# Performance work log

Measured on AMD Instinct MI355X. Metric: run time of the kernel, lower is better.

Reference implementation:

```python
import jax, jax.numpy as jnp
import numpy as np

D_MODEL = 1024
NHEADS = 16
E_HEAD = D_MODEL // NHEADS  # 64
ROPE_BASE = 10000.0


def _rope_cos_sin(L, dim, base, dtype):
    # dim = E_head (even); inv_freq over pairs, GPT-NeoX half-split convention
    inv_freq = 1.0 / (base ** (jnp.arange(0, dim, 2, dtype=jnp.float32) / dim))
    pos = jnp.arange(L, dtype=jnp.float32)
    freqs = pos[:, None] * inv_freq[None, :]  # [L, dim/2]
    return jnp.cos(freqs).astype(dtype), jnp.sin(freqs).astype(dtype)


def _apply_rope(t, cos, sin):
    # t: [B, H, L, Dh]; rotate-half formulation
    d2 = t.shape[-1] // 2
    t1, t2 = t[..., :d2], t[..., d2:]
    return jnp.concatenate([t1 * cos - t2 * sin, t1 * sin + t2 * cos], axis=-1)


def setup_inputs() -> dict:
    key = jax.random.key(0)
    ks = jax.random.split(key, 5)
    B, L = 4, 2048
    x = jax.random.normal(ks[0], (B, L, D_MODEL), dtype=jnp.float32)
    s_in = 1.0 / np.sqrt(D_MODEL)
    W_packed = jax.random.normal(ks[1], (3 * D_MODEL, D_MODEL), dtype=jnp.float32) * s_in
    b_packed = jax.random.normal(ks[2], (3 * D_MODEL,), dtype=jnp.float32) * 0.02
    W_out = jax.random.normal(ks[3], (D_MODEL, D_MODEL), dtype=jnp.float32) * s_in
    b_out = jax.random.normal(ks[4], (D_MODEL,), dtype=jnp.float32) * 0.02
    return {"x": x, "W_packed": W_packed, "b_packed": b_packed, "W_out": W_out, "b_out": b_out}


def reference(x, W_packed, b_packed, W_out, b_out):
    B, L, _ = x.shape
    # 1) packed QKV projection (query is key is value path)
    qkv = jnp.einsum('ble,fe->blf', x, W_packed) + b_packed  # [B, L, 3*D]
    q, k, v = jnp.split(qkv, 3, axis=-1)
    # 2) split heads -> [B, H, L, Dh]
    def heads(t):
        return t.reshape(B, L, NHEADS, E_HEAD).transpose(0, 2, 1, 3)
    q, k, v = heads(q), heads(k), heads(v)
    # 3) RoPE on q, k
    cos, sin = _rope_cos_sin(L, E_HEAD, ROPE_BASE, x.dtype)
    q = _apply_rope(q, cos, sin)
    k = _apply_rope(k, cos, sin)
    # 4) SDPA (non-causal, no dropout)
    scale = 1.0 / np.sqrt(E_HEAD)
    scores = jnp.einsum('bhqd,bhkd->bhqk', q, k) * scale
    attn = jax.nn.softmax(scores, axis=-1)
    out = jnp.einsum('bhqk,bhkd->bhqd', attn, v)
    # 5) merge heads + output projection
    out = out.transpose(0, 2, 1, 3).reshape(B, L, D_MODEL)
    return jnp.einsum('bld,ed->ble', out, W_out) + b_out
```

## Files before the change

kernel.cpp:

```cpp
#include <hip/hip_runtime.h>
#include <hip/hip_bf16.h>
#include <stdint.h>

#define L_SEQ 2048
#define NB    4
#define NH    16
#define EH    64
#define DM    1024
#define MTOT  (NB * L_SEQ)

typedef __attribute__((ext_vector_type(8))) short bf16x8;
typedef __attribute__((ext_vector_type(4))) float f32x4;
typedef __attribute__((ext_vector_type(16))) float f32x16;

static __device__ __forceinline__ float bf2f(short u) {
    union { unsigned int i; float f; } c;
    c.i = ((unsigned int)(unsigned short)u) << 16;
    return c.f;
}
static __device__ __forceinline__ short f2bf(float f) {
    union { float f; unsigned int i; } c; c.f = f;
    unsigned int x = c.i;
    unsigned int r = (x + 0x7fffu + ((x >> 16) & 1u)) >> 16;
    return (short)(unsigned short)r;
}
static __device__ __forceinline__ unsigned cvtpk(float lo, float hi) {
    unsigned r;
    asm volatile("v_cvt_pk_bf16_f32 %0, %1, %2" : "=v"(r) : "v"(lo), "v"(hi));
    return r;
}

static __device__ __forceinline__ void gload_lds16(const void* g, void* lds) {
    __builtin_amdgcn_global_load_lds(
        (const __attribute__((address_space(1))) unsigned int*)g,
        (__attribute__((address_space(3))) unsigned int*)lds, 16, 0, 0);
}

__global__ __launch_bounds__(256) void cvt3_k(const float* __restrict__ x,
                                              const float* __restrict__ wp,
                                              const float* __restrict__ wo,
                                              short* __restrict__ xb,
                                              short* __restrict__ wpb,
                                              short* __restrict__ wob,
                                              float* __restrict__ tab) {
    int bid = blockIdx.x;
    if (bid >= 12288) {
        int i = (bid - 12288) * 256 + threadIdx.x;
        int l = i >> 5, d = i & 31;
        float inv = powf(10000.0f, -(float)d * (1.0f / 32.0f));
        float fr = (float)l * inv;
        tab[i]         = cosf(fr);
        tab[65536 + i] = sinf(fr);
        return;
    }
    const float* src; short* dst; int i;
    if (bid < 8192)       { src = x;  dst = xb;  i = bid * 256 + threadIdx.x; }
    else if (bid < 11264) { src = wp; dst = wpb; i = (bid - 8192) * 256 + threadIdx.x; }
    else                  { src = wo; dst = wob; i = (bid - 11264) * 256 + threadIdx.x; }
    float4 v = ((const float4*)src)[i];
    short4 o;
    o.x = f2bf(v.x); o.y = f2bf(v.y); o.z = f2bf(v.z); o.w = f2bf(v.w);
    ((short4*)dst)[i] = o;
}

template<int OUTBF16, int NBN, int NCOL>
__global__ __launch_bounds__(512, 2) void gemmA_k(const short* __restrict__ A,
                                                  const short* __restrict__ Bt,
                                                  const float* __restrict__ bias,
                                                  void* __restrict__ Cv) {
    __shared__ short lds[2][384 * 32];
    const int t = threadIdx.x;
    const int w = t >> 6, l = t & 63;
    const int wm = w >> 1, wn = w & 1;
    const int lr = l & 15, lh = l >> 4;

    const int nblk = NBN * 32;
    int fid = blockIdx.x + blockIdx.y * NBN;
    int swz = (fid & 7) * (nblk >> 3) + (fid >> 3);
    const int n0 = (swz % NBN) * 128;
    const int m0 = (swz / NBN) * 256;

    const int lrow = l >> 2;
    const int schunk = (l & 3) ^ ((l >> 3) & 3);

    const short* Ag = A + (size_t)(m0 + lrow) * 1024 + schunk * 8;
    const short* Bg = Bt + (size_t)(n0 + lrow) * 1024 + schunk * 8;

    auto STAGE = [&](int kt, int buf) {
        gload_lds16(Ag + (size_t)(w * 32) * 1024 + kt * 32,      &lds[buf][(w * 32) * 32]);
        gload_lds16(Ag + (size_t)(w * 32 + 16) * 1024 + kt * 32, &lds[buf][(w * 32 + 16) * 32]);
        gload_lds16(Bg + (size_t)(w * 16) * 1024 + kt * 32,      &lds[buf][8192 + (w * 16) * 32]);
    };

    f32x4 acc[4][4] = {};

    STAGE(0, 0);
    STAGE(1, 1);
    asm volatile("s_waitcnt vmcnt(3)" ::: "memory");
    __builtin_amdgcn_s_barrier();

    const int fch = (lh ^ ((lr >> 1) & 3)) << 3;

#pragma unroll 2
    for (int kt = 0; kt < 32; ++kt) {
        const int c = kt & 1;
        const short* Al = &lds[c][0];
        const short* Bl = &lds[c][8192];

        bf16x8 bfr[4], af[4];
#pragma unroll
        for (int nj = 0; nj < 4; ++nj)
            bfr[nj] = *(const bf16x8*)(Bl + (wn * 64 + nj * 16 + lr) * 32 + fch);
#pragma unroll
        for (int mi = 0; mi < 4; ++mi)
            af[mi] = *(const bf16x8*)(Al + (wm * 64 + mi * 16 + lr) * 32 + fch);

        __builtin_amdgcn_s_setprio(1);
#pragma unroll
        for (int mi = 0; mi < 4; ++mi)
#pragma unroll
            for (int nj = 0; nj < 4; ++nj)
                acc[mi][nj] = __builtin_amdgcn_mfma_f32_16x16x32_bf16(
                    af[mi], bfr[nj], acc[mi][nj], 0, 0, 0);
        __builtin_amdgcn_s_setprio(0);

        asm volatile("s_waitcnt lgkmcnt(0)" ::: "memory");
        __builtin_amdgcn_s_barrier();
        if (kt + 2 < 32) {
            STAGE(kt + 2, c);
            asm volatile("s_waitcnt vmcnt(3)" ::: "memory");
        } else {
            asm volatile("s_waitcnt vmcnt(0)" ::: "memory");
        }
        __builtin_amdgcn_s_barrier();
    }

#pragma unroll
    for (int mi = 0; mi < 4; ++mi) {
#pragma unroll
        for (int nj = 0; nj < 4; ++nj) {
            const int row = m0 + wm * 64 + mi * 16 + lh * 4;
            const int col = n0 + wn * 64 + nj * 16 + lr;
            const float bsv = bias[col];
#pragma unroll
            for (int j = 0; j < 4; ++j) {
                float v = acc[mi][nj][j] + bsv;
                if (OUTBF16)
                    ((short*)Cv)[(size_t)(row + j) * NCOL + col] = f2bf(v);
                else
                    ((float*)Cv)[(size_t)(row + j) * NCOL + col] = v;
            }
        }
    }
}

__global__ __launch_bounds__(256) void scatter_k(const short* __restrict__ qkv,
                                                 const float* __restrict__ tab,
                                                 short* __restrict__ Q,
                                                 short* __restrict__ Kd,
                                                 short* __restrict__ Vt) {
    int bid = blockIdx.x;
    if (bid < 4096) {
        int idx = bid * 256 + threadIdx.x;
        int dp = (idx & 7) * 4;
        int h = (idx >> 3) & 15;
        int bl = idx >> 7;
        int l = bl & (L_SEQ - 1);
        int b = bl >> 11;
        float4 cs = *(const float4*)&tab[l * 32 + dp];
        float4 sn = *(const float4*)&tab[65536 + l * 32 + dp];
        const short* row = qkv + (size_t)bl * 3072;
        size_t ob = ((size_t)((b * 16 + h) * 2048 + l)) * 64;
        const float sc = 0.18033688011112042f;
        short4 q1 = *(const short4*)&row[h * 64 + dp];
        short4 q2 = *(const short4*)&row[h * 64 + dp + 32];
        union { unsigned u[2]; short4 s4; } a1, a2;
        a1.u[0] = cvtpk((bf2f(q1.x) * cs.x - bf2f(q2.x) * sn.x) * sc,
                        (bf2f(q1.y) * cs.y - bf2f(q2.y) * sn.y) * sc);
        a1.u[1] = cvtpk((bf2f(q1.z) * cs.z - bf2f(q2.z) * sn.z) * sc,
                        (bf2f(q1.w) * cs.w - bf2f(q2.w) * sn.w) * sc);
        a2.u[0] = cvtpk((bf2f(q1.x) * sn.x + bf2f(q2.x) * cs.x) * sc,
                        (bf2f(q1.y) * sn.y + bf2f(q2.y) * cs.y) * sc);
        a2.u[1] = cvtpk((bf2f(q1.z) * sn.z + bf2f(q2.z) * cs.z) * sc,
                        (bf2f(q1.w) * sn.w + bf2f(q2.w) * cs.w) * sc);
        *(short4*)(Q + ob + dp)      = a1.s4;
        *(short4*)(Q + ob + dp + 32) = a2.s4;
        short4 k1 = *(const short4*)&row[1024 + h * 64 + dp];
        short4 k2 = *(const short4*)&row[1024 + h * 64 + dp + 32];
        union { unsigned u[2]; short4 s4; } e1, e2;
        e1.u[0] = cvtpk(bf2f(k1.x) * cs.x - bf2f(k2.x) * sn.x,
                        bf2f(k1.y) * cs.y - bf2f(k2.y) * sn.y);
        e1.u[1] = cvtpk(bf2f(k1.z) * cs.z - bf2f(k2.z) * sn.z,
                        bf2f(k1.w) * cs.w - bf2f(k2.w) * sn.w);
        e2.u[0] = cvtpk(bf2f(k1.x) * sn.x + bf2f(k2.x) * cs.x,
                        bf2f(k1.y) * sn.y + bf2f(k2.y) * cs.y);
        e2.u[1] = cvtpk(bf2f(k1.z) * sn.z + bf2f(k2.z) * cs.z,
                        bf2f(k1.w) * sn.w + bf2f(k2.w) * cs.w);
        int r7 = l & 7;
        int c1 = ((dp >> 3) ^ r7) * 8 + (dp & 7);
        int c2 = (((dp >> 3) | 4) ^ r7) * 8 + (dp & 7);
        *(short4*)(Kd + ob + c1) = e1.s4;
        *(short4*)(Kd + ob + c2) = e2.s4;
        return;
    }
    __shared__ short tile[64 * 65];
    int bid2 = bid - 4096;
    int l0 = (bid2 & 31) * 64;
    int bh = bid2 >> 5;
    int t = threadIdx.x;
    int b = bh >> 4, h = bh & 15;
#pragma unroll
    for (int i = 0; i < 16; i++) {
        int l = i * 4 + (t >> 6);
        int d = t & 63;
        tile[d * 65 + l] = qkv[(size_t)(b * 2048 + l0 + l) * 3072 + 2048 + h * 64 + d];
    }
    __syncthreads();
#pragma unroll
    for (int i = 0; i < 16; i++) {
        int d = i * 4 + (t >> 6);
        int lx = t & 63;
        int cl = (lx & ~0xC) | ((lx & 4) << 1) | ((lx & 8) >> 1);
        int lp = l0 | ((((cl >> 3) ^ (d & 7)) << 3)) | (cl & 7);
        Vt[(size_t)(bh * 64 + d) * 2048 + lp] = tile[d * 65 + lx];
    }
}

__global__ __launch_bounds__(512, 2) void attn_k(const short* __restrict__ Qg,
                                                 const short* __restrict__ Kg,
                                                 const short* __restrict__ Vt,
                                                 short* __restrict__ O) {
    __shared__ short Ks[3][64 * 64];
    __shared__ short Vs[3][64 * 64];
    const int t = threadIdx.x;
    const int w = t >> 6, l = t & 63;
    const int q = l & 31, hi = l >> 5;
    const int r7 = l & 7;

    const int od = blockIdx.x + blockIdx.y * 8;
    const int qblk = (od >> 3) & 7;
    const int bh = (od & 7) * 8 + (od >> 6);
    const int q0 = qblk * 256;

    const short* Qb = Qg + (size_t)bh * (2048 * 64);
    const short* Kb = Kg + (size_t)bh * (2048 * 64);
    const short* Vb = Vt + (size_t)bh * (64 * 2048);

    const int qrow = q0 + w * 32 + q;
    bf16x8 qf[4];
#pragma unroll
    for (int ds = 0; ds < 4; ds++)
        qf[ds] = *(const bf16x8*)(Qb + (size_t)qrow * 64 + ds * 16 + hi * 8);

    const short one_bf = (short)0x3F80;
    const bf16x8 ones = {one_bf, one_bf, one_bf, one_bf, one_bf, one_bf, one_bf, one_bf};

    f32x16 o0 = {}, o1 = {}, os = {};

    const int grow = w * 8 + (l >> 3);
    const int gcol = r7 * 8;

    gload_lds16(Kb + (size_t)grow * 64 + gcol,        &Ks[0][w * 512]);
    gload_lds16(Vb + (size_t)grow * 2048 + gcol,      &Vs[0][w * 512]);
    gload_lds16(Kb + (size_t)(64 + grow) * 64 + gcol, &Ks[1][w * 512]);
    gload_lds16(Vb + (size_t)grow * 2048 + 64 + gcol, &Vs[1][w * 512]);
    asm volatile("s_waitcnt vmcnt(2)" ::: "memory");
    __builtin_amdgcn_s_barrier();

    const short* Kc = &Ks[0][0];  const short* Vc = &Vs[0][0];
    const short* Kn = &Ks[1][0];  const short* Vn = &Vs[1][0];
    short*       Kf = &Ks[2][0];  short*       Vf = &Vs[2][0];

    for (int it = 0; it < 32; ++it) {
        if (it < 30) {
            const int kn = (it + 2) * 64;
            gload_lds16(Kb + (size_t)(kn + grow) * 64 + gcol, Kf + w * 512);
            gload_lds16(Vb + (size_t)grow * 2048 + kn + gcol, Vf + w * 512);
        }

        f32x16 s0 = {}, s1 = {};
#pragma unroll
        for (int ds = 0; ds < 4; ds++) {
            const int ch = ((ds << 1) | hi) ^ r7;
            bf16x8 k0f = *(const bf16x8*)(Kc + q * 64 + ch * 8);
            bf16x8 k1f = *(const bf16x8*)(Kc + (32 + q) * 64 + ch * 8);
            __builtin_amdgcn_s_setprio(1);
            s0 = __builtin_amdgcn_mfma_f32_32x32x16_bf16(k0f, qf[ds], s0, 0, 0, 0);
            s1 = __builtin_amdgcn_mfma_f32_32x32x16_bf16(k1f, qf[ds], s1, 0, 0, 0);
            __builtin_amdgcn_s_setprio(0);
        }

#pragma unroll
        for (int r = 0; r < 16; r++) {
            s0[r] = __builtin_amdgcn_exp2f(s0[r]);
            s1[r] = __builtin_amdgcn_exp2f(s1[r]);
        }

        bf16x8 pf[4];
        {
            union { unsigned u[4]; bf16x8 v; } f;
            f.u[0] = cvtpk(s0[0], s0[1]);  f.u[1] = cvtpk(s0[2], s0[3]);
            f.u[2] = cvtpk(s0[4], s0[5]);  f.u[3] = cvtpk(s0[6], s0[7]);
            pf[0] = f.v;
            f.u[0] = cvtpk(s0[8], s0[9]);  f.u[1] = cvtpk(s0[10], s0[11]);
            f.u[2] = cvtpk(s0[12], s0[13]); f.u[3] = cvtpk(s0[14], s0[15]);
            pf[1] = f.v;
            f.u[0] = cvtpk(s1[0], s1[1]);  f.u[1] = cvtpk(s1[2], s1[3]);
            f.u[2] = cvtpk(s1[4], s1[5]);  f.u[3] = cvtpk(s1[6], s1[7]);
            pf[2] = f.v;
            f.u[0] = cvtpk(s1[8], s1[9]);  f.u[1] = cvtpk(s1[10], s1[11]);
            f.u[2] = cvtpk(s1[12], s1[13]); f.u[3] = cvtpk(s1[14], s1[15]);
            pf[3] = f.v;
        }

#pragma unroll
        for (int ks = 0; ks < 4; ks++) {
            const int ch = ((ks << 1) | hi) ^ r7;
            bf16x8 v0f = *(const bf16x8*)(Vc + q * 64 + ch * 8);
            bf16x8 v1f = *(const bf16x8*)(Vc + (32 + q) * 64 + ch * 8);
            __builtin_amdgcn_s_setprio(1);
            o0 = __builtin_amdgcn_mfma_f32_32x32x16_bf16(v0f, pf[ks], o0, 0, 0, 0);
            o1 = __builtin_amdgcn_mfma_f32_32x32x16_bf16(v1f, pf[ks], o1, 0, 0, 0);
            os = __builtin_amdgcn_mfma_f32_32x32x16_bf16(ones, pf[ks], os, 0, 0, 0);
            __builtin_amdgcn_s_setprio(0);
        }

        asm volatile("s_waitcnt lgkmcnt(0)" ::: "memory");
        if (it < 30) asm volatile("s_waitcnt vmcnt(2)" ::: "memory");
        else         asm volatile("s_waitcnt vmcnt(0)" ::: "memory");
        __builtin_amdgcn_s_barrier();

        const short* tk = Kc; Kc = Kn; Kn = Kf; Kf = (short*)tk;
        const short* tv = Vc; Vc = Vn; Vn = Vf; Vf = (short*)tv;
    }

    const float inv = 1.0f / os[0];
    const int b = bh >> 4, h = bh & 15;
    short* Orow = O + (size_t)(b * 2048 + qrow) * 1024 + h * 64;
#pragma unroll
    for (int g = 0; g < 4; g++) {
        unsigned w0 = cvtpk(o0[g * 4 + 0] * inv, o0[g * 4 + 1] * inv);
        unsigned w1 = cvtpk(o0[g * 4 + 2] * inv, o0[g * 4 + 3] * inv);
        unsigned long long p0 = (unsigned long long)w0 | ((unsigned long long)w1 << 32);
        *(unsigned long long*)(Orow + g * 8 + hi * 4) = p0;
        unsigned w2 = cvtpk(o1[g * 4 + 0] * inv, o1[g * 4 + 1] * inv);
        unsigned w3 = cvtpk(o1[g * 4 + 2] * inv, o1[g * 4 + 3] * inv);
        unsigned long long p1 = (unsigned long long)w2 | ((unsigned long long)w3 << 32);
        *(unsigned long long*)(Orow + 32 + g * 8 + hi * 4) = p1;
    }
}

extern "C" void kernel_launch(void* const* d_in, const int* in_sizes, int n_in,
                              void* d_out, int out_size, void* d_ws, size_t ws_size,
                              hipStream_t stream) {
    const float* x  = (const float*)d_in[0];
    const float* Wp = (const float*)d_in[1];
    const float* bp = (const float*)d_in[2];
    const float* Wo = (const float*)d_in[3];
    const float* bo = (const float*)d_in[4];

    char* ws = (char*)d_ws;
    const size_t SZ_XB  = (size_t)MTOT * DM * 2;
    const size_t SZ_WPB = (size_t)3 * DM * DM * 2;
    const size_t SZ_WOB = (size_t)DM * DM * 2;
    const size_t SZ_QKV = (size_t)MTOT * 3 * DM * 2;
    const size_t SZ_BHLE = (size_t)MTOT * DM * 2;

    short* xb   = (short*)(ws);
    short* wpb  = (short*)(ws + SZ_XB);
    short* wob  = (short*)(ws + SZ_XB + SZ_WPB);
    short* qkvb = (short*)(ws + SZ_XB + SZ_WPB + SZ_WOB);
    short* Qb   = (short*)(ws + SZ_XB + SZ_WPB + SZ_WOB + SZ_QKV);
    short* Kb   = (short*)(ws + SZ_XB + SZ_WPB + SZ_WOB + SZ_QKV + SZ_BHLE);
    short* Vtb  = (short*)(ws + SZ_XB + SZ_WPB + SZ_WOB + SZ_QKV + 2 * SZ_BHLE);
    short* Ob   = (short*)(ws + SZ_XB + SZ_WPB + SZ_WOB + SZ_QKV + 3 * SZ_BHLE);
    float* tab  = (float*)(ws + SZ_XB + SZ_WPB + SZ_WOB + SZ_QKV + 4 * SZ_BHLE);

    cvt3_k<<<12544, 256, 0, stream>>>(x, Wp, Wo, xb, wpb, wob, tab);

    gemmA_k<1, 24, 3072><<<dim3(24, 32), 512, 0, stream>>>(xb, wpb, bp, qkvb);

    scatter_k<<<6144, 256, 0, stream>>>(qkvb, tab, Qb, Kb, Vtb);

    attn_k<<<dim3(8, 64), 512, 0, stream>>>(Qb, Kb, Vtb, Ob);

    gemmA_k<0, 8, 1024><<<dim3(8, 32), 512, 0, stream>>>(Ob, wob, bo, (float*)d_out);
}
```

Baseline: 191.4 us.

## Fuse head-split scatter into QKV GEMM epilogue and apply Q RoPE in attention

The QKV GEMM now writes Q and K directly in head-major layout and V transposed and swizzled, so the intermediate packed QKV buffer and the scatter/transpose kernel go away. RoPE for Q moves into the attention kernel's Q load, using a new transposed cos/sin table. RoPE for K stays in a smaller separate kernel. This removes a full round trip of the QKV tensor through global memory. In exchange the GEMM epilogue does scattered short stores and the attention prologue does extra table loads.

```diff
diff --git a/kernel.cpp b/kernel.cpp
--- a/kernel.cpp
+++ b/kernel.cpp
@@ -42,8 +42,18 @@
                                               short* __restrict__ xb,
                                               short* __restrict__ wpb,
                                               short* __restrict__ wob,
-                                              float* __restrict__ tab) {
+                                              float* __restrict__ tab,
+                                              float* __restrict__ tabT) {
     int bid = blockIdx.x;
+    if (bid >= 12544) {
+        int i = (bid - 12544) * 256 + threadIdx.x;
+        int di = i >> 11, l = i & 2047;
+        float inv = powf(10000.0f, -(float)di * (1.0f / 32.0f));
+        float fr = (float)l * inv;
+        tabT[i]         = cosf(fr);
+        tabT[65536 + i] = sinf(fr);
+        return;
+    }
     if (bid >= 12288) {
         int i = (bid - 12288) * 256 + threadIdx.x;
         int l = i >> 5, d = i & 31;
@@ -63,11 +73,14 @@
     ((short4*)dst)[i] = o;
 }
 
-template<int OUTBF16, int NBN, int NCOL>
+template<int OUTBF16, int NBN, int NCOL, int EPI>
 __global__ __launch_bounds__(512, 2) void gemmA_k(const short* __restrict__ A,
                                                   const short* __restrict__ Bt,
                                                   const float* __restrict__ bias,
-                                                  void* __restrict__ Cv) {
+                                                  void* __restrict__ Cv,
+                                                  short* __restrict__ Qp,
+                                                  short* __restrict__ Kp,
+                                                  short* __restrict__ Vt) {
     __shared__ short lds[2][384 * 32];
     const int t = threadIdx.x;
     const int w = t >> 6, l = t & 63;
@@ -135,100 +148,94 @@
         __builtin_amdgcn_s_barrier();
     }
 
-#pragma unroll
-    for (int mi = 0; mi < 4; ++mi) {
-#pragma unroll
-        for (int nj = 0; nj < 4; ++nj) {
-            const int row = m0 + wm * 64 + mi * 16 + lh * 4;
-            const int col = n0 + wn * 64 + nj * 16 + lr;
-            const float bsv = bias[col];
-#pragma unroll
-            for (int j = 0; j < 4; ++j) {
-                float v = acc[mi][nj][j] + bsv;
-                if (OUTBF16)
-                    ((short*)Cv)[(size_t)(row + j) * NCOL + col] = f2bf(v);
-                else
-                    ((float*)Cv)[(size_t)(row + j) * NCOL + col] = v;
+    if (EPI == 0) {
+#pragma unroll
+        for (int mi = 0; mi < 4; ++mi) {
+#pragma unroll
+            for (int nj = 0; nj < 4; ++nj) {
+                const int row = m0 + wm * 64 + mi * 16 + lh * 4;
+                const int col = n0 + wn * 64 + nj * 16 + lr;
+                const float bsv = bias[col];
+#pragma unroll
+                for (int j = 0; j < 4; ++j) {
+                    float v = acc[mi][nj][j] + bsv;
+                    if (OUTBF16)
+                        ((short*)Cv)[(size_t)(row + j) * NCOL + col] = f2bf(v);
+                    else
+                        ((float*)Cv)[(size_t)(row + j) * NCOL + col] = v;
+                }
             }
         }
-    }
-}
-
-__global__ __launch_bounds__(256) void scatter_k(const short* __restrict__ qkv,
-                                                 const float* __restrict__ tab,
-                                                 short* __restrict__ Q,
-                                                 short* __restrict__ Kd,
-                                                 short* __restrict__ Vt) {
-    int bid = blockIdx.x;
-    if (bid < 4096) {
-        int idx = bid * 256 + threadIdx.x;
-        int dp = (idx & 7) * 4;
-        int h = (idx >> 3) & 15;
-        int bl = idx >> 7;
-        int l = bl & (L_SEQ - 1);
-        int b = bl >> 11;
-        float4 cs = *(const float4*)&tab[l * 32 + dp];
-        float4 sn = *(const float4*)&tab[65536 + l * 32 + dp];
-        const short* row = qkv + (size_t)bl * 3072;
-        size_t ob = ((size_t)((b * 16 + h) * 2048 + l)) * 64;
-        const float sc = 0.18033688011112042f;
-        short4 q1 = *(const short4*)&row[h * 64 + dp];
-        short4 q2 = *(const short4*)&row[h * 64 + dp + 32];
-        union { unsigned u[2]; short4 s4; } a1, a2;
-        a1.u[0] = cvtpk((bf2f(q1.x) * cs.x - bf2f(q2.x) * sn.x) * sc,
-                        (bf2f(q1.y) * cs.y - bf2f(q2.y) * sn.y) * sc);
-        a1.u[1] = cvtpk((bf2f(q1.z) * cs.z - bf2f(q2.z) * sn.z) * sc,
-                        (bf2f(q1.w) * cs.w - bf2f(q2.w) * sn.w) * sc);
-        a2.u[0] = cvtpk((bf2f(q1.x) * sn.x + bf2f(q2.x) * cs.x) * sc,
-                        (bf2f(q1.y) * sn.y + bf2f(q2.y) * cs.y) * sc);
-        a2.u[1] = cvtpk((bf2f(q1.z) * sn.z + bf2f(q2.z) * cs.z) * sc,
-                        (bf2f(q1.w) * sn.w + bf2f(q2.w) * cs.w) * sc);
-        *(short4*)(Q + ob + dp)      = a1.s4;
-        *(short4*)(Q + ob + dp + 32) = a2.s4;
-        short4 k1 = *(const short4*)&row[1024 + h * 64 + dp];
-        short4 k2 = *(const short4*)&row[1024 + h * 64 + dp + 32];
-        union { unsigned u[2]; short4 s4; } e1, e2;
-        e1.u[0] = cvtpk(bf2f(k1.x) * cs.x - bf2f(k2.x) * sn.x,
-                        bf2f(k1.y) * cs.y - bf2f(k2.y) * sn.y);
-        e1.u[1] = cvtpk(bf2f(k1.z) * cs.z - bf2f(k2.z) * sn.z,
-                        bf2f(k1.w) * cs.w - bf2f(k2.w) * sn.w);
-        e2.u[0] = cvtpk(bf2f(k1.x) * sn.x + bf2f(k2.x) * cs.x,
-                        bf2f(k1.y) * sn.y + bf2f(k2.y) * cs.y);
-        e2.u[1] = cvtpk(bf2f(k1.z) * sn.z + bf2f(k2.z) * cs.z,
-                        bf2f(k1.w) * sn.w + bf2f(k2.w) * cs.w);
-        int r7 = l & 7;
-        int c1 = ((dp >> 3) ^ r7) * 8 + (dp & 7);
-        int c2 = (((dp >> 3) | 4) ^ r7) * 8 + (dp & 7);
-        *(short4*)(Kd + ob + c1) = e1.s4;
-        *(short4*)(Kd + ob + c2) = e2.s4;
-        return;
-    }
-    __shared__ short tile[64 * 65];
-    int bid2 = bid - 4096;
-    int l0 = (bid2 & 31) * 64;
-    int bh = bid2 >> 5;
-    int t = threadIdx.x;
-    int b = bh >> 4, h = bh & 15;
-#pragma unroll
-    for (int i = 0; i < 16; i++) {
-        int l = i * 4 + (t >> 6);
-        int d = t & 63;
-        tile[d * 65 + l] = qkv[(size_t)(b * 2048 + l0 + l) * 3072 + 2048 + h * 64 + d];
-    }
-    __syncthreads();
-#pragma unroll
-    for (int i = 0; i < 16; i++) {
-        int d = i * 4 + (t >> 6);
-        int lx = t & 63;
-        int cl = (lx & ~0xC) | ((lx & 4) << 1) | ((lx & 8) >> 1);
-        int lp = l0 | ((((cl >> 3) ^ (d & 7)) << 3)) | (cl & 7);
-        Vt[(size_t)(bh * 64 + d) * 2048 + lp] = tile[d * 65 + lx];
-    }
-}
-
-__global__ __launch_bounds__(512, 2) void attn_k(const short* __restrict__ Qg,
+    } else {
+        const int part = n0 >> 10;
+        const int h = ((n0 & 1023) >> 6) + wn;
+#pragma unroll
+        for (int mi = 0; mi < 4; ++mi) {
+            const int r0 = m0 + wm * 64 + mi * 16 + lh * 4;
+            const int bq = r0 >> 11, lq = r0 & 2047;
+            if (part < 2) {
+                short* Drow = (part == 0 ? Qp : Kp) + ((size_t)(bq * 16 + h) * 2048 + lq) * 64;
+#pragma unroll
+                for (int nj = 0; nj < 4; ++nj) {
+                    const int d = nj * 16 + lr;
+                    const float bsv = bias[n0 + wn * 64 + d];
+#pragma unroll
+                    for (int j = 0; j < 4; ++j)
+                        Drow[j * 64 + d] = f2bf(acc[mi][nj][j] + bsv);
+                }
+            } else {
+                const int lpb = (lq & ~63) + (((mi * 2 + (lh & 1)) ^ (lr & 7)) << 3) + ((lh >> 1) * 4);
+#pragma unroll
+                for (int nj = 0; nj < 4; ++nj) {
+                    const int d = nj * 16 + lr;
+                    const float bsv = bias[n0 + wn * 64 + d];
+                    short4 sv;
+                    sv.x = f2bf(acc[mi][nj][0] + bsv);
+                    sv.y = f2bf(acc[mi][nj][1] + bsv);
+                    sv.z = f2bf(acc[mi][nj][2] + bsv);
+                    sv.w = f2bf(acc[mi][nj][3] + bsv);
+                    *(short4*)(Vt + (size_t)((bq * 16 + h) * 64 + d) * 2048 + lpb) = sv;
+                }
+            }
+        }
+    }
+}
+
+__global__ __launch_bounds__(256) void krope_k(const short* __restrict__ Kpre,
+                                               const float* __restrict__ tab,
+                                               short* __restrict__ Kd) {
+    int idx = blockIdx.x * 256 + threadIdx.x;
+    int dp = (idx & 7) * 4;
+    int h = (idx >> 3) & 15;
+    int bl = idx >> 7;
+    int l = bl & (L_SEQ - 1);
+    int b = bl >> 11;
+    float4 cs = *(const float4*)&tab[l * 32 + dp];
+    float4 sn = *(const float4*)&tab[65536 + l * 32 + dp];
+    size_t ob = ((size_t)((b * 16 + h) * 2048 + l)) * 64;
+    const short* src = Kpre + ob;
+    short4 k1 = *(const short4*)&src[dp];
+    short4 k2 = *(const short4*)&src[dp + 32];
+    union { unsigned u[2]; short4 s4; } e1, e2;
+    e1.u[0] = cvtpk(bf2f(k1.x) * cs.x - bf2f(k2.x) * sn.x,
+                    bf2f(k1.y) * cs.y - bf2f(k2.y) * sn.y);
+    e1.u[1] = cvtpk(bf2f(k1.z) * cs.z - bf2f(k2.z) * sn.z,
+                    bf2f(k1.w) * cs.w - bf2f(k2.w) * sn.w);
+    e2.u[0] = cvtpk(bf2f(k1.x) * sn.x + bf2f(k2.x) * cs.x,
+                    bf2f(k1.y) * sn.y + bf2f(k2.y) * cs.y);
+    e2.u[1] = cvtpk(bf2f(k1.z) * sn.z + bf2f(k2.z) * cs.z,
+                    bf2f(k1.w) * sn.w + bf2f(k2.w) * cs.w);
+    int r7 = l & 7;
+    int c1 = ((dp >> 3) ^ r7) * 8 + (dp & 7);
+    int c2 = (((dp >> 3) | 4) ^ r7) * 8 + (dp & 7);
+    *(short4*)(Kd + ob + c1) = e1.s4;
+    *(short4*)(Kd + ob + c2) = e2.s4;
+}
+
+__global__ __launch_bounds__(512, 2) void attn_k(const short* __restrict__ Qpre,
                                                  const short* __restrict__ Kg,
                                                  const short* __restrict__ Vt,
+                                                 const float* __restrict__ tabT,
                                                  short* __restrict__ O) {
     __shared__ short Ks[3][64 * 64];
     __shared__ short Vs[3][64 * 64];
@@ -242,15 +249,35 @@
     const int bh = (od & 7) * 8 + (od >> 6);
     const int q0 = qblk * 256;
 
-    const short* Qb = Qg + (size_t)bh * (2048 * 64);
     const short* Kb = Kg + (size_t)bh * (2048 * 64);
     const short* Vb = Vt + (size_t)bh * (64 * 2048);
 
     const int qrow = q0 + w * 32 + q;
+
+    const short* Qsrc = Qpre + (size_t)bh * (2048 * 64) + (size_t)qrow * 64;
+    bf16x8 qraw[4];
+#pragma unroll
+    for (int ds = 0; ds < 4; ds++)
+        qraw[ds] = *(const bf16x8*)(Qsrc + ds * 16 + hi * 8);
+    const float sc = 0.18033688011112042f;
     bf16x8 qf[4];
 #pragma unroll
-    for (int ds = 0; ds < 4; ds++)
-        qf[ds] = *(const bf16x8*)(Qb + (size_t)qrow * 64 + ds * 16 + hi * 8);
+    for (int dsL = 0; dsL < 2; dsL++) {
+        union { unsigned u[4]; bf16x8 v; } lo, hg;
+#pragma unroll
+        for (int p = 0; p < 4; p++) {
+            const int d0 = dsL * 16 + hi * 8 + 2 * p;
+            float c0 = tabT[d0 * 2048 + qrow];
+            float s0 = tabT[65536 + d0 * 2048 + qrow];
+            float c1 = tabT[(d0 + 1) * 2048 + qrow];
+            float s1 = tabT[65536 + (d0 + 1) * 2048 + qrow];
+            float a0 = bf2f(qraw[dsL][2 * p]),     b0 = bf2f(qraw[dsL + 2][2 * p]);
+            float a1 = bf2f(qraw[dsL][2 * p + 1]), b1 = bf2f(qraw[dsL + 2][2 * p + 1]);
+            lo.u[p] = cvtpk((a0 * c0 - b0 * s0) * sc, (a1 * c1 - b1 * s1) * sc);
+            hg.u[p] = cvtpk((a0 * s0 + b0 * c0) * sc, (a1 * s1 + b1 * c1) * sc);
+        }
+        qf[dsL] = lo.v; qf[dsL + 2] = hg.v;
+    }
 
     const short one_bf = (short)0x3F80;
     const bf16x8 ones = {one_bf, one_bf, one_bf, one_bf, one_bf, one_bf, one_bf, one_bf};
@@ -363,26 +390,29 @@
     const size_t SZ_XB  = (size_t)MTOT * DM * 2;
     const size_t SZ_WPB = (size_t)3 * DM * DM * 2;
     const size_t SZ_WOB = (size_t)DM * DM * 2;
-    const size_t SZ_QKV = (size_t)MTOT * 3 * DM * 2;
     const size_t SZ_BHLE = (size_t)MTOT * DM * 2;
+    const size_t SZ_TAB = (size_t)131072 * 4;
 
     short* xb   = (short*)(ws);
     short* wpb  = (short*)(ws + SZ_XB);
     short* wob  = (short*)(ws + SZ_XB + SZ_WPB);
-    short* qkvb = (short*)(ws + SZ_XB + SZ_WPB + SZ_WOB);
-    short* Qb   = (short*)(ws + SZ_XB + SZ_WPB + SZ_WOB + SZ_QKV);
-    short* Kb   = (short*)(ws + SZ_XB + SZ_WPB + SZ_WOB + SZ_QKV + SZ_BHLE);
-    short* Vtb  = (short*)(ws + SZ_XB + SZ_WPB + SZ_WOB + SZ_QKV + 2 * SZ_BHLE);
-    short* Ob   = (short*)(ws + SZ_XB + SZ_WPB + SZ_WOB + SZ_QKV + 3 * SZ_BHLE);
-    float* tab  = (float*)(ws + SZ_XB + SZ_WPB + SZ_WOB + SZ_QKV + 4 * SZ_BHLE);
-
-    cvt3_k<<<12544, 256, 0, stream>>>(x, Wp, Wo, xb, wpb, wob, tab);
-
-    gemmA_k<1, 24, 3072><<<dim3(24, 32), 512, 0, stream>>>(xb, wpb, bp, qkvb);
-
-    scatter_k<<<6144, 256, 0, stream>>>(qkvb, tab, Qb, Kb, Vtb);
-
-    attn_k<<<dim3(8, 64), 512, 0, stream>>>(Qb, Kb, Vtb, Ob);
-
-    gemmA_k<0, 8, 1024><<<dim3(8, 32), 512, 0, stream>>>(Ob, wob, bo, (float*)d_out);
-}
+    short* Qpre = (short*)(ws + SZ_XB + SZ_WPB + SZ_WOB);
+    short* Kpre = (short*)(ws + SZ_XB + SZ_WPB + SZ_WOB + SZ_BHLE);
+    short* Kb   = (short*)(ws + SZ_XB + SZ_WPB + SZ_WOB + 2 * SZ_BHLE);
+    short* Vtb  = (short*)(ws + SZ_XB + SZ_WPB + SZ_WOB + 3 * SZ_BHLE);
+    short* Ob   = (short*)(ws + SZ_XB + SZ_WPB + SZ_WOB + 4 * SZ_BHLE);
+    float* tab  = (float*)(ws + SZ_XB + SZ_WPB + SZ_WOB + 5 * SZ_BHLE);
+    float* tabT = (float*)(ws + SZ_XB + SZ_WPB + SZ_WOB + 5 * SZ_BHLE + SZ_TAB);
+
+    cvt3_k<<<12800, 256, 0, stream>>>(x, Wp, Wo, xb, wpb, wob, tab, tabT);
+
+    gemmA_k<1, 24, 3072, 1><<<dim3(24, 32), 512, 0, stream>>>(
+        xb, wpb, bp, nullptr, Qpre, Kpre, Vtb);
+
+    krope_k<<<4096, 256, 0, stream>>>(Kpre, tab, Kb);
+
+    attn_k<<<dim3(8, 64), 512, 0, stream>>>(Qpre, Kb, Vtb, tabT, Ob);
+
+    gemmA_k<0, 8, 1024, 0><<<dim3(8, 32), 512, 0, stream>>>(
+        Ob, wob, bo, (float*)d_out, nullptr, nullptr, nullptr);
+}
```

Result: faster. 185.5 us (-3.1%).
